# Kernel optimization log

Measured on AMD Instinct MI355X. Metric: run time of the kernel, lower is better.

## Reference

```python
import jax, jax.numpy as jnp
import numpy as np

D_MODEL = 1024
NUM_HEADS = 16
D_K = D_MODEL // NUM_HEADS


def setup_inputs() -> dict:
    key = jax.random.key(0)
    ks = jax.random.split(key, 12)
    B, T = 2, 2048
    s = 1.0 / np.sqrt(D_MODEL)
    inp = {
        "q": jax.random.normal(ks[0], (B, T, D_MODEL), jnp.float32),
        "k": jax.random.normal(ks[1], (B, T, D_MODEL), jnp.float32),
        "v": jax.random.normal(ks[2], (B, T, D_MODEL), jnp.float32),
        "mask": jnp.ones((B, 1, 1, T), dtype=bool),
        "Wq": jax.random.normal(ks[3], (D_MODEL, D_MODEL), jnp.float32) * s,
        "bq": jnp.zeros((D_MODEL,), jnp.float32),
        "Wk": jax.random.normal(ks[4], (D_MODEL, D_MODEL), jnp.float32) * s,
        "bk": jnp.zeros((D_MODEL,), jnp.float32),
        "Wv": jax.random.normal(ks[5], (D_MODEL, D_MODEL), jnp.float32) * s,
        "bv": jnp.zeros((D_MODEL,), jnp.float32),
        "Wo": jax.random.normal(ks[6], (D_MODEL, D_MODEL), jnp.float32) * s,
        "bo": jnp.zeros((D_MODEL,), jnp.float32),
    }
    return inp


def _split_heads(x):
    # (B, T, d_model) -> (B, H, T, d_k)
    B, T, _ = x.shape
    return x.reshape(B, T, NUM_HEADS, D_K).transpose(0, 2, 1, 3)


def reference(q, k, v, mask, Wq, bq, Wk, bk, Wv, bv, Wo, bo):
    B, Tq, _ = q.shape
    qh = _split_heads(q @ Wq + bq)   # (B,H,Tq,dk)
    kh = _split_heads(k @ Wk + bk)   # (B,H,Tk,dk)
    vh = _split_heads(v @ Wv + bv)   # (B,H,Tk,dk)
    scores = jnp.einsum("bhqd,bhkd->bhqk", qh, kh) / jnp.sqrt(jnp.float32(D_K))
    scores = jnp.where(mask, scores, -jnp.inf)
    attn = jax.nn.softmax(scores.astype(jnp.float32), axis=-1).astype(scores.dtype)
    # dropout is identity in eval mode
    out = jnp.einsum("bhqk,bhkd->bhqd", attn, vh)
    out = out.transpose(0, 2, 1, 3).reshape(B, Tq, D_MODEL)
    return out @ Wo + bo
```

## Files before the change

kernel.cpp:

```cpp
#include <hip/hip_runtime.h>
#include <hip/hip_bf16.h>


#define T_      2048
#define DMODEL  1024
#define NH      16
#define DK      64

typedef __attribute__((ext_vector_type(8))) short   bf16x8;
typedef __attribute__((ext_vector_type(4))) float   f32x4;
typedef __attribute__((ext_vector_type(4))) unsigned short u16x4;
typedef __attribute__((ext_vector_type(8))) unsigned short u16x8;

static __device__ __forceinline__ unsigned short f2bf(float f) {
    union { float f; unsigned u; } v; v.f = f;
    unsigned r = (v.u + 0x7fffu + ((v.u >> 16) & 1u)) >> 16;
    return (unsigned short)r;
}

static __device__ __forceinline__ void gld16(const unsigned short* g,
                                             unsigned short* l) {
    __builtin_amdgcn_global_load_lds(
        (const __attribute__((address_space(1))) unsigned int*)(const void*)g,
        (__attribute__((address_space(3))) unsigned int*)(void*)l, 16, 0, 0);
}

__global__ __launch_bounds__(256) void cast_x(
        const float* __restrict__ q, const float* __restrict__ k,
        const float* __restrict__ v, unsigned short* __restrict__ Xb) {
    const float* src = (blockIdx.y == 0) ? q : (blockIdx.y == 1) ? k : v;
    unsigned short* d = Xb + (size_t)blockIdx.y * (4096u * 1024u);
    size_t i = ((size_t)blockIdx.x * 256 + threadIdx.x) * 4;
    float4 vv = *reinterpret_cast<const float4*>(src + i);
    u16x4 o;
    o[0] = f2bf(vv.x); o[1] = f2bf(vv.y); o[2] = f2bf(vv.z); o[3] = f2bf(vv.w);
    *reinterpret_cast<u16x4*>(d + i) = o;
}

__global__ __launch_bounds__(256) void cast_wt(
        const float* __restrict__ Wq, const float* __restrict__ Wk,
        const float* __restrict__ Wv, const float* __restrict__ Wo,
        unsigned short* __restrict__ dst) {
    __shared__ unsigned short Ls[64][68];
    const float* src = (blockIdx.z == 0) ? Wq : (blockIdx.z == 1) ? Wk
                     : (blockIdx.z == 2) ? Wv : Wo;
    unsigned short* d = dst + (size_t)blockIdx.z * (1024u * 1024u);
    const int k0 = blockIdx.y * 64, n0 = blockIdx.x * 64;
    const int tid = threadIdx.x;
    #pragma unroll
    for (int i = 0; i < 4; i++) {
        int g = tid + i * 256;
        int r = g >> 4, c = (g & 15) * 4;
        float4 v = *reinterpret_cast<const float4*>(
            src + (size_t)(k0 + r) * 1024 + n0 + c);
        u16x4 o;
        o[0] = f2bf(v.x); o[1] = f2bf(v.y); o[2] = f2bf(v.z); o[3] = f2bf(v.w);
        *reinterpret_cast<u16x4*>(&Ls[r][c]) = o;
    }
    __syncthreads();
    #pragma unroll
    for (int i = 0; i < 4; i++) {
        int g = tid + i * 256;
        int n = g >> 4, kq = (g & 15) * 4;
        u16x4 o;
        #pragma unroll
        for (int j = 0; j < 4; j++) o[j] = Ls[kq + j][n];
        *reinterpret_cast<u16x4*>(d + (size_t)(n0 + n) * 1024 + k0 + kq) = o;
    }
}

#define CSCALE 0.18033688011112042f
#define CLD 136

__global__ __launch_bounds__(256) void qkv_gemm(
        const unsigned short* __restrict__ Xb,
        const unsigned short* __restrict__ Wt,
        const float* __restrict__ bq, const float* __restrict__ bk,
        const float* __restrict__ bv,
        unsigned short* __restrict__ Qh, unsigned short* __restrict__ Kf,
        unsigned short* __restrict__ Vf) {
    __shared__ unsigned short Al[128 * 32];
    __shared__ unsigned short Bl[128 * 32];
    __shared__ unsigned short Cl[128 * CLD];
    const int z = blockIdx.z;
    const unsigned short* X = Xb + (size_t)z * (4096u * 1024u);
    const unsigned short* W = Wt + (size_t)z * (1024u * 1024u);
    const float* bias = (z == 0) ? bq : (z == 1) ? bk : bv;
    const float oscale = (z == 0) ? CSCALE : 1.0f;

    const int tid  = threadIdx.x;
    const int lane = tid & 63, w = tid >> 6;
    const int quad = lane >> 4, l16 = lane & 15;
    const int row0 = blockIdx.y * 128, n0 = blockIdx.x * 128;
    const int wm = w >> 1, wn = w & 1;

    const int srow = w * 32 + (lane >> 2);
    const int scol = (lane & 3) * 8;
    const unsigned short* gA0 = X + (size_t)(row0 + srow) * 1024 + scol;
    const unsigned short* gA1 = gA0 + (size_t)16 * 1024;
    const unsigned short* gB0 = W + (size_t)(n0 + srow) * 1024 + scol;
    const unsigned short* gB1 = gB0 + (size_t)16 * 1024;
    unsigned short* lA0 = &Al[w * 1024];
    unsigned short* lA1 = &Al[w * 1024 + 512];
    unsigned short* lB0 = &Bl[w * 1024];
    unsigned short* lB1 = &Bl[w * 1024 + 512];

    f32x4 acc[4][4];
    for (int mt = 0; mt < 4; mt++)
        for (int nt = 0; nt < 4; nt++)
            acc[mt][nt] = (f32x4){0.f, 0.f, 0.f, 0.f};

    for (int k0 = 0; k0 < 1024; k0 += 32) {
        gld16(gA0 + k0, lA0);
        gld16(gA1 + k0, lA1);
        gld16(gB0 + k0, lB0);
        gld16(gB1 + k0, lB1);
        __syncthreads();
        bf16x8 a[4], b[4];
        #pragma unroll
        for (int mt = 0; mt < 4; mt++)
            a[mt] = *reinterpret_cast<const bf16x8*>(
                &Al[(wm * 64 + mt * 16 + l16) * 32 + quad * 8]);
        #pragma unroll
        for (int nt = 0; nt < 4; nt++)
            b[nt] = *reinterpret_cast<const bf16x8*>(
                &Bl[(wn * 64 + nt * 16 + l16) * 32 + quad * 8]);
        #pragma unroll
        for (int mt = 0; mt < 4; mt++)
            #pragma unroll
            for (int nt = 0; nt < 4; nt++)
                acc[mt][nt] = __builtin_amdgcn_mfma_f32_16x16x32_bf16(
                    a[mt], b[nt], acc[mt][nt], 0, 0, 0);
        __syncthreads();
    }

    #pragma unroll
    for (int mt = 0; mt < 4; mt++) {
        int row = wm * 64 + mt * 16 + quad * 4;
        #pragma unroll
        for (int nt = 0; nt < 4; nt++) {
            int col = wn * 64 + nt * 16 + l16;
            float bvv = bias[n0 + col];
            #pragma unroll
            for (int r = 0; r < 4; r++)
                Cl[(row + r) * CLD + col] = f2bf((acc[mt][nt][r] + bvv) * oscale);
        }
    }
    __syncthreads();

    const int bb = row0 >> 11;
    const int T0 = (row0 & 2047) >> 7;
    const int h0 = n0 >> 6;

    if (z == 0) {
        #pragma unroll
        for (int i = 0; i < 8; i++) {
            int c = tid + i * 256;
            int row = c >> 4, cc = (c & 15) * 8;
            int col = n0 + cc;
            int h = col >> 6, d = col & 63;
            int t = (row0 + row) & 2047;
            u16x8 vv = *reinterpret_cast<const u16x8*>(&Cl[row * CLD + cc]);
            *reinterpret_cast<u16x8*>(
                Qh + ((size_t)(bb * NH + h) * T_ + t) * DK + d) = vv;
        }
    } else if (z == 1) {
        #pragma unroll
        for (int i = 0; i < 8; i++) {
            int c = tid + i * 256;
            int hh = c >> 10;
            int nt = (c >> 7) & 7, kt = (c >> 6) & 1;
            int q4 = (c >> 4) & 3, lc = c & 15;
            int koff = (nt & 3) * 32 + (nt >> 2) * 4 + (lc >> 2) * 8 + (lc & 3);
            u16x8 vv = *reinterpret_cast<const u16x8*>(
                &Cl[koff * CLD + hh * 64 + kt * 32 + q4 * 8]);
            size_t base = ((size_t)((bb * NH + h0 + hh) * 16 + T0)) * 8192;
            *reinterpret_cast<u16x8*>(
                Kf + base + nt * 1024 + kt * 512 + q4 * 128 + lc * 8) = vv;
        }
    } else {
        #pragma unroll
        for (int i = 0; i < 8; i++) {
            int c = tid + i * 256;
            int hh = c >> 10;
            int kk = (c >> 8) & 3, nt = (c >> 6) & 3;
            int q4 = (c >> 4) & 3, lc = c & 15;
            int colc = hh * 64 + nt * 16 + lc;
            u16x8 vv;
            #pragma unroll
            for (int j = 0; j < 8; j++)
                vv[j] = Cl[(kk * 32 + q4 * 8 + j) * CLD + colc];
            size_t base = ((size_t)((bb * NH + h0 + hh) * 16 + T0)) * 8192;
            *reinterpret_cast<u16x8*>(
                Vf + base + kk * 2048 + nt * 512 + q4 * 128 + lc * 8) = vv;
        }
    }
}

__global__ __launch_bounds__(256, 4) void flash_attn(
        const unsigned short* __restrict__ Qh,
        const unsigned short* __restrict__ Kf,
        const unsigned short* __restrict__ Vf,
        float* __restrict__ Opart, float* __restrict__ Lpart) {
    __shared__ __attribute__((aligned(16))) unsigned short KV[16384];
    const int tid  = threadIdx.x;
    const int lane = tid & 63;
    const int w = tid >> 6;
    const int quad = lane >> 4, l16 = lane & 15;
    const int bh = blockIdx.y, b = bh >> 4, h = bh & 15;
    const int z = blockIdx.z;
    const int qrow = blockIdx.x * 128 + w * 32;
    const unsigned short* Qp = Qh + (size_t)bh * T_ * DK;
    float* Op = Opart + (size_t)z * 4096 * 1024;
    float* Lp = Lpart + (size_t)z * 32 * T_ + (size_t)bh * T_;

    bf16x8 qa[2][2];
    #pragma unroll
    for (int mt = 0; mt < 2; mt++)
        #pragma unroll
        for (int kt = 0; kt < 2; kt++)
            qa[mt][kt] = *reinterpret_cast<const bf16x8*>(
                Qp + (size_t)(qrow + mt * 16 + l16) * DK + kt * 32 + quad * 8);

    f32x4 o[2][4];
    float lsum[2] = {0.f, 0.f};
    #pragma unroll
    for (int mt = 0; mt < 2; mt++)
        #pragma unroll
        for (int nt = 0; nt < 4; nt++) o[mt][nt] = (f32x4){0.f, 0.f, 0.f, 0.f};

    const int halfsel = (w >> 1);
    unsigned short* lbase = &KV[halfsel * 8192 + (w & 1) * 4096];
    const size_t fragoff = ((w & 1) * 512) * 8 + (size_t)lane * 8;

    for (int it = 0; it < 8; it++) {
        const int T0 = z * 8 + it;
        const size_t winbase = ((size_t)(bh * 16 + T0)) * 8192;
        const unsigned short* gsrc =
            (halfsel == 0 ? Kf : Vf) + winbase + fragoff;
        __syncthreads();
        #pragma unroll
        for (int i = 0; i < 8; i++)
            gld16(gsrc + i * 512, lbase + i * 512);
        asm volatile("s_waitcnt vmcnt(0)" ::: "memory");
        __syncthreads();

        f32x4 s[2][8];
        #pragma unroll
        for (int nt = 0; nt < 8; nt++) {
            s[0][nt] = (f32x4){0.f, 0.f, 0.f, 0.f};
            s[1][nt] = (f32x4){0.f, 0.f, 0.f, 0.f};
        }
        #pragma unroll
        for (int nt = 0; nt < 8; nt++)
            #pragma unroll
            for (int kt = 0; kt < 2; kt++) {
                bf16x8 kbv = *reinterpret_cast<const bf16x8*>(
                    &KV[nt * 1024 + kt * 512 + lane * 8]);
                s[0][nt] = __builtin_amdgcn_mfma_f32_16x16x32_bf16(
                    kbv, qa[0][kt], s[0][nt], 0, 0, 0);
                s[1][nt] = __builtin_amdgcn_mfma_f32_16x16x32_bf16(
                    kbv, qa[1][kt], s[1][nt], 0, 0, 0);
            }

        int pk[2][16];
        #pragma unroll
        for (int mt = 0; mt < 2; mt++) {
            float lloc = 0.f;
            #pragma unroll
            for (int nt = 0; nt < 8; nt++) {
                float e0 = exp2f(s[mt][nt][0]);
                float e1 = exp2f(s[mt][nt][1]);
                float e2 = exp2f(s[mt][nt][2]);
                float e3 = exp2f(s[mt][nt][3]);
                int p0 = __builtin_amdgcn_perm(__float_as_int(e1),
                                               __float_as_int(e0), 0x07060302);
                int p1 = __builtin_amdgcn_perm(__float_as_int(e3),
                                               __float_as_int(e2), 0x07060302);
                pk[mt][nt * 2]     = p0;
                pk[mt][nt * 2 + 1] = p1;
                lloc += __int_as_float(p0 << 16) + __int_as_float(p0 & 0xffff0000)
                      + __int_as_float(p1 << 16) + __int_as_float(p1 & 0xffff0000);
            }
            lsum[mt] += lloc;
        }

        #pragma unroll
        for (int kt = 0; kt < 4; kt++) {
            union { int i[4]; bf16x8 v; } pu0, pu1;
            pu0.i[0] = pk[0][kt * 2];     pu0.i[1] = pk[0][kt * 2 + 1];
            pu0.i[2] = pk[0][kt * 2 + 8]; pu0.i[3] = pk[0][kt * 2 + 9];
            pu1.i[0] = pk[1][kt * 2];     pu1.i[1] = pk[1][kt * 2 + 1];
            pu1.i[2] = pk[1][kt * 2 + 8]; pu1.i[3] = pk[1][kt * 2 + 9];
            #pragma unroll
            for (int nt = 0; nt < 4; nt++) {
                bf16x8 vbv = *reinterpret_cast<const bf16x8*>(
                    &KV[8192 + kt * 2048 + nt * 512 + lane * 8]);
                o[0][nt] = __builtin_amdgcn_mfma_f32_16x16x32_bf16(
                    pu0.v, vbv, o[0][nt], 0, 0, 0);
                o[1][nt] = __builtin_amdgcn_mfma_f32_16x16x32_bf16(
                    pu1.v, vbv, o[1][nt], 0, 0, 0);
            }
        }
    }

    #pragma unroll
    for (int mt = 0; mt < 2; mt++) {
        float lf = lsum[mt];
        lf += __shfl_xor(lf, 16);
        lf += __shfl_xor(lf, 32);
        if (quad == 0) Lp[qrow + mt * 16 + l16] = lf;
        int t = qrow + mt * 16 + quad * 4;
        #pragma unroll
        for (int nt = 0; nt < 4; nt++) {
            int d = nt * 16 + l16;
            #pragma unroll
            for (int r = 0; r < 4; r++)
                Op[((size_t)(b * T_ + t + r)) * DMODEL + h * DK + d] = o[mt][nt][r];
        }
    }
}

__global__ __launch_bounds__(256) void combine(
        const float* __restrict__ O, const float* __restrict__ L,
        unsigned short* __restrict__ ctx) {
    size_t gid = (size_t)blockIdx.x * 256 + threadIdx.x;
    int row = (int)(gid >> 8);
    int c4  = (int)(gid & 255);
    int h = c4 >> 4;
    int b = row >> 11, t = row & 2047;
    size_t li = ((size_t)(b * 16 + h)) * T_ + t;
    float inv = 1.f / (L[li] + L[li + 32 * T_]);
    size_t oi = (size_t)row * 1024 + c4 * 4;
    float4 a  = *reinterpret_cast<const float4*>(O + oi);
    float4 c  = *reinterpret_cast<const float4*>(O + (size_t)4096 * 1024 + oi);
    u16x4 o;
    o[0] = f2bf((a.x + c.x) * inv);
    o[1] = f2bf((a.y + c.y) * inv);
    o[2] = f2bf((a.z + c.z) * inv);
    o[3] = f2bf((a.w + c.w) * inv);
    *reinterpret_cast<u16x4*>(ctx + oi) = o;
}

__global__ __launch_bounds__(256) void out_gemm(
        const unsigned short* __restrict__ A, const unsigned short* __restrict__ Wt,
        const float* __restrict__ bias, float* __restrict__ out) {
    __shared__ unsigned short Al[64 * 32];
    __shared__ unsigned short Bl[128 * 32];
    const int tid  = threadIdx.x;
    const int lane = tid & 63, w = tid >> 6;
    const int quad = lane >> 4, l16 = lane & 15;
    const int row0 = blockIdx.y * 64, n0 = blockIdx.x * 128;
    const int wm = w >> 1, wn = w & 1;

    const int scol = (lane & 3) * 8;
    const unsigned short* gA0 = A + (size_t)(row0 + w * 16 + (lane >> 2)) * 1024 + scol;
    const unsigned short* gB0 = Wt + (size_t)(n0 + w * 32 + (lane >> 2)) * 1024 + scol;
    const unsigned short* gB1 = gB0 + (size_t)16 * 1024;
    unsigned short* lA0 = &Al[w * 512];
    unsigned short* lB0 = &Bl[w * 1024];
    unsigned short* lB1 = &Bl[w * 1024 + 512];

    f32x4 acc[2][4];
    for (int mt = 0; mt < 2; mt++)
        for (int nt = 0; nt < 4; nt++)
            acc[mt][nt] = (f32x4){0.f, 0.f, 0.f, 0.f};

    for (int k0 = 0; k0 < 1024; k0 += 32) {
        gld16(gA0 + k0, lA0);
        gld16(gB0 + k0, lB0);
        gld16(gB1 + k0, lB1);
        __syncthreads();
        bf16x8 a[2], b[4];
        #pragma unroll
        for (int mt = 0; mt < 2; mt++)
            a[mt] = *reinterpret_cast<const bf16x8*>(
                &Al[(wm * 32 + mt * 16 + l16) * 32 + quad * 8]);
        #pragma unroll
        for (int nt = 0; nt < 4; nt++)
            b[nt] = *reinterpret_cast<const bf16x8*>(
                &Bl[(wn * 64 + nt * 16 + l16) * 32 + quad * 8]);
        #pragma unroll
        for (int mt = 0; mt < 2; mt++)
            #pragma unroll
            for (int nt = 0; nt < 4; nt++)
                acc[mt][nt] = __builtin_amdgcn_mfma_f32_16x16x32_bf16(
                    a[mt], b[nt], acc[mt][nt], 0, 0, 0);
        __syncthreads();
    }

    #pragma unroll
    for (int mt = 0; mt < 2; mt++) {
        int rowb = row0 + wm * 32 + mt * 16 + quad * 4;
        #pragma unroll
        for (int nt = 0; nt < 4; nt++) {
            int col = n0 + wn * 64 + nt * 16 + l16;
            float bvv = bias[col];
            #pragma unroll
            for (int r = 0; r < 4; r++)
                out[(size_t)(rowb + r) * 1024 + col] = acc[mt][nt][r] + bvv;
        }
    }
}

extern "C" void kernel_launch(void* const* d_in, const int* in_sizes, int n_in,
                              void* d_out, int out_size, void* d_ws, size_t ws_size,
                              hipStream_t stream) {
    const float* q  = (const float*)d_in[0];
    const float* k  = (const float*)d_in[1];
    const float* v  = (const float*)d_in[2];
    const float* Wq = (const float*)d_in[4];
    const float* bq = (const float*)d_in[5];
    const float* Wk = (const float*)d_in[6];
    const float* bk = (const float*)d_in[7];
    const float* Wv = (const float*)d_in[8];
    const float* bv = (const float*)d_in[9];
    const float* Wo = (const float*)d_in[10];
    const float* bo = (const float*)d_in[11];
    float* out = (float*)d_out;

    unsigned short* ws  = (unsigned short*)d_ws;
    unsigned short* Wt  = ws;
    unsigned short* Qh  = ws + (size_t)4  * 1024 * 1024;
    unsigned short* Kf  = ws + (size_t)8  * 1024 * 1024;
    unsigned short* Vf  = ws + (size_t)12 * 1024 * 1024;
    unsigned short* Xb  = ws + (size_t)16 * 1024 * 1024;
    float* Opart = (float*)(ws + (size_t)16 * 1024 * 1024);
    float* Lpart = (float*)(ws + (size_t)32 * 1024 * 1024);
    unsigned short* ctx = Kf;

    cast_x <<<dim3(4096, 3), 256, 0, stream>>>(q, k, v, Xb);
    cast_wt<<<dim3(16, 16, 4), 256, 0, stream>>>(Wq, Wk, Wv, Wo, Wt);
    qkv_gemm<<<dim3(8, 32, 3), 256, 0, stream>>>(Xb, Wt, bq, bk, bv, Qh, Kf, Vf);
    flash_attn<<<dim3(16, 32, 2), 256, 0, stream>>>(Qh, Kf, Vf, Opart, Lpart);
    combine<<<dim3(4096), 256, 0, stream>>>(Opart, Lpart, ctx);
    out_gemm<<<dim3(8, 64), 256, 0, stream>>>(ctx, Wt + (size_t)3 * 1048576, bo, out);
}
```

Before: 246.2 us.

## Fuse cast kernels, fold split-K combine into output GEMM, MFMA row sums

Merges the activation and weight cast kernels into one launch, removes the separate combine kernel by having the output GEMM read both fp32 partial outputs, normalise by the inverse denominator and convert to bf16 while staging its A tile, and computes the softmax denominator in flash attention with an MFMA against a ones vector instead of scalar adds and shuffles. The aim is to cut launches and the ctx round-trip through global memory. In exchange, the out GEMM now reads fp32 partials directly, 8x per column tile (eight column blocks reread the same rows), so it moves more data than the bf16 ctx it replaces.

```diff
diff --git a/kernel.cpp b/kernel.cpp
--- a/kernel.cpp
+++ b/kernel.cpp
@@ -25,47 +25,50 @@
         (__attribute__((address_space(3))) unsigned int*)(void*)l, 16, 0, 0);
 }
 
-__global__ __launch_bounds__(256) void cast_x(
+__global__ __launch_bounds__(256) void prep(
         const float* __restrict__ q, const float* __restrict__ k,
-        const float* __restrict__ v, unsigned short* __restrict__ Xb) {
-    const float* src = (blockIdx.y == 0) ? q : (blockIdx.y == 1) ? k : v;
-    unsigned short* d = Xb + (size_t)blockIdx.y * (4096u * 1024u);
-    size_t i = ((size_t)blockIdx.x * 256 + threadIdx.x) * 4;
-    float4 vv = *reinterpret_cast<const float4*>(src + i);
-    u16x4 o;
-    o[0] = f2bf(vv.x); o[1] = f2bf(vv.y); o[2] = f2bf(vv.z); o[3] = f2bf(vv.w);
-    *reinterpret_cast<u16x4*>(d + i) = o;
-}
-
-__global__ __launch_bounds__(256) void cast_wt(
+        const float* __restrict__ v,
         const float* __restrict__ Wq, const float* __restrict__ Wk,
         const float* __restrict__ Wv, const float* __restrict__ Wo,
-        unsigned short* __restrict__ dst) {
+        unsigned short* __restrict__ Xb, unsigned short* __restrict__ Wt) {
     __shared__ unsigned short Ls[64][68];
-    const float* src = (blockIdx.z == 0) ? Wq : (blockIdx.z == 1) ? Wk
-                     : (blockIdx.z == 2) ? Wv : Wo;
-    unsigned short* d = dst + (size_t)blockIdx.z * (1024u * 1024u);
-    const int k0 = blockIdx.y * 64, n0 = blockIdx.x * 64;
-    const int tid = threadIdx.x;
-    #pragma unroll
-    for (int i = 0; i < 4; i++) {
-        int g = tid + i * 256;
-        int r = g >> 4, c = (g & 15) * 4;
-        float4 v = *reinterpret_cast<const float4*>(
-            src + (size_t)(k0 + r) * 1024 + n0 + c);
+    const int bx = blockIdx.x, tid = threadIdx.x;
+    if (bx < 12288) {
+        int y = bx >> 12, sub = bx & 4095;
+        const float* src = (y == 0) ? q : (y == 1) ? k : v;
+        unsigned short* d = Xb + (size_t)y * (4096u * 1024u);
+        size_t i = ((size_t)sub * 256 + tid) * 4;
+        float4 vv = *reinterpret_cast<const float4*>(src + i);
         u16x4 o;
-        o[0] = f2bf(v.x); o[1] = f2bf(v.y); o[2] = f2bf(v.z); o[3] = f2bf(v.w);
-        *reinterpret_cast<u16x4*>(&Ls[r][c]) = o;
-    }
-    __syncthreads();
-    #pragma unroll
-    for (int i = 0; i < 4; i++) {
-        int g = tid + i * 256;
-        int n = g >> 4, kq = (g & 15) * 4;
-        u16x4 o;
-        #pragma unroll
-        for (int j = 0; j < 4; j++) o[j] = Ls[kq + j][n];
-        *reinterpret_cast<u16x4*>(d + (size_t)(n0 + n) * 1024 + k0 + kq) = o;
+        o[0] = f2bf(vv.x); o[1] = f2bf(vv.y); o[2] = f2bf(vv.z); o[3] = f2bf(vv.w);
+        *reinterpret_cast<u16x4*>(d + i) = o;
+    } else {
+        int bxx = bx - 12288;
+        int zz = bxx >> 8, rem = bxx & 255;
+        int k0 = (rem >> 4) * 64, n0 = (rem & 15) * 64;
+        const float* src = (zz == 0) ? Wq : (zz == 1) ? Wk
+                         : (zz == 2) ? Wv : Wo;
+        unsigned short* d = Wt + (size_t)zz * (1024u * 1024u);
+        #pragma unroll
+        for (int i = 0; i < 4; i++) {
+            int g = tid + i * 256;
+            int r = g >> 4, c = (g & 15) * 4;
+            float4 vv = *reinterpret_cast<const float4*>(
+                src + (size_t)(k0 + r) * 1024 + n0 + c);
+            u16x4 o;
+            o[0] = f2bf(vv.x); o[1] = f2bf(vv.y); o[2] = f2bf(vv.z); o[3] = f2bf(vv.w);
+            *reinterpret_cast<u16x4*>(&Ls[r][c]) = o;
+        }
+        __syncthreads();
+        #pragma unroll
+        for (int i = 0; i < 4; i++) {
+            int g = tid + i * 256;
+            int n = g >> 4, kq = (g & 15) * 4;
+            u16x4 o;
+            #pragma unroll
+            for (int j = 0; j < 4; j++) o[j] = Ls[kq + j][n];
+            *reinterpret_cast<u16x4*>(d + (size_t)(n0 + n) * 1024 + k0 + kq) = o;
+        }
     }
 }
 
@@ -222,12 +225,16 @@
             qa[mt][kt] = *reinterpret_cast<const bf16x8*>(
                 Qp + (size_t)(qrow + mt * 16 + l16) * DK + kt * 32 + quad * 8);
 
-    f32x4 o[2][4];
-    float lsum[2] = {0.f, 0.f};
-    #pragma unroll
-    for (int mt = 0; mt < 2; mt++)
+    f32x4 o[2][4], lden[2];
+    #pragma unroll
+    for (int mt = 0; mt < 2; mt++) {
+        lden[mt] = (f32x4){0.f, 0.f, 0.f, 0.f};
         #pragma unroll
         for (int nt = 0; nt < 4; nt++) o[mt][nt] = (f32x4){0.f, 0.f, 0.f, 0.f};
+    }
+
+    union { unsigned u[4]; bf16x8 v; } ones;
+    ones.u[0] = ones.u[1] = ones.u[2] = ones.u[3] = 0x3F803F80u;
 
     const int halfsel = (w >> 1);
     unsigned short* lbase = &KV[halfsel * 8192 + (w & 1) * 4096];
@@ -265,25 +272,18 @@
 
         int pk[2][16];
         #pragma unroll
-        for (int mt = 0; mt < 2; mt++) {
-            float lloc = 0.f;
+        for (int mt = 0; mt < 2; mt++)
             #pragma unroll
             for (int nt = 0; nt < 8; nt++) {
                 float e0 = exp2f(s[mt][nt][0]);
                 float e1 = exp2f(s[mt][nt][1]);
                 float e2 = exp2f(s[mt][nt][2]);
                 float e3 = exp2f(s[mt][nt][3]);
-                int p0 = __builtin_amdgcn_perm(__float_as_int(e1),
-                                               __float_as_int(e0), 0x07060302);
-                int p1 = __builtin_amdgcn_perm(__float_as_int(e3),
-                                               __float_as_int(e2), 0x07060302);
-                pk[mt][nt * 2]     = p0;
-                pk[mt][nt * 2 + 1] = p1;
-                lloc += __int_as_float(p0 << 16) + __int_as_float(p0 & 0xffff0000)
-                      + __int_as_float(p1 << 16) + __int_as_float(p1 & 0xffff0000);
+                pk[mt][nt * 2] = __builtin_amdgcn_perm(
+                    __float_as_int(e1), __float_as_int(e0), 0x07060302);
+                pk[mt][nt * 2 + 1] = __builtin_amdgcn_perm(
+                    __float_as_int(e3), __float_as_int(e2), 0x07060302);
             }
-            lsum[mt] += lloc;
-        }
 
         #pragma unroll
         for (int kt = 0; kt < 4; kt++) {
@@ -301,15 +301,20 @@
                 o[1][nt] = __builtin_amdgcn_mfma_f32_16x16x32_bf16(
                     pu1.v, vbv, o[1][nt], 0, 0, 0);
             }
+            lden[0] = __builtin_amdgcn_mfma_f32_16x16x32_bf16(
+                pu0.v, ones.v, lden[0], 0, 0, 0);
+            lden[1] = __builtin_amdgcn_mfma_f32_16x16x32_bf16(
+                pu1.v, ones.v, lden[1], 0, 0, 0);
         }
     }
 
     #pragma unroll
     for (int mt = 0; mt < 2; mt++) {
-        float lf = lsum[mt];
-        lf += __shfl_xor(lf, 16);
-        lf += __shfl_xor(lf, 32);
-        if (quad == 0) Lp[qrow + mt * 16 + l16] = lf;
+        if (l16 == 0) {
+            #pragma unroll
+            for (int r = 0; r < 4; r++)
+                Lp[qrow + mt * 16 + quad * 4 + r] = lden[mt][r];
+        }
         int t = qrow + mt * 16 + quad * 4;
         #pragma unroll
         for (int nt = 0; nt < 4; nt++) {
@@ -321,43 +326,34 @@
     }
 }
 
-__global__ __launch_bounds__(256) void combine(
-        const float* __restrict__ O, const float* __restrict__ L,
-        unsigned short* __restrict__ ctx) {
-    size_t gid = (size_t)blockIdx.x * 256 + threadIdx.x;
-    int row = (int)(gid >> 8);
-    int c4  = (int)(gid & 255);
-    int h = c4 >> 4;
-    int b = row >> 11, t = row & 2047;
-    size_t li = ((size_t)(b * 16 + h)) * T_ + t;
-    float inv = 1.f / (L[li] + L[li + 32 * T_]);
-    size_t oi = (size_t)row * 1024 + c4 * 4;
-    float4 a  = *reinterpret_cast<const float4*>(O + oi);
-    float4 c  = *reinterpret_cast<const float4*>(O + (size_t)4096 * 1024 + oi);
-    u16x4 o;
-    o[0] = f2bf((a.x + c.x) * inv);
-    o[1] = f2bf((a.y + c.y) * inv);
-    o[2] = f2bf((a.z + c.z) * inv);
-    o[3] = f2bf((a.w + c.w) * inv);
-    *reinterpret_cast<u16x4*>(ctx + oi) = o;
-}
-
 __global__ __launch_bounds__(256) void out_gemm(
-        const unsigned short* __restrict__ A, const unsigned short* __restrict__ Wt,
+        const float* __restrict__ Opart, const float* __restrict__ Lpart,
+        const unsigned short* __restrict__ Wt,
         const float* __restrict__ bias, float* __restrict__ out) {
     __shared__ unsigned short Al[64 * 32];
     __shared__ unsigned short Bl[128 * 32];
+    __shared__ float invs[64 * 16];
     const int tid  = threadIdx.x;
     const int lane = tid & 63, w = tid >> 6;
     const int quad = lane >> 4, l16 = lane & 15;
     const int row0 = blockIdx.y * 64, n0 = blockIdx.x * 128;
     const int wm = w >> 1, wn = w & 1;
 
+    #pragma unroll
+    for (int i = 0; i < 4; i++) {
+        int e = tid + i * 256;
+        int row = e >> 4, hh = e & 15;
+        int rg = row0 + row, bb = rg >> 11, tt = rg & 2047;
+        size_t li = ((size_t)(bb * NH + hh)) * T_ + tt;
+        invs[e] = 1.f / (Lpart[li] + Lpart[li + 32 * T_]);
+    }
+
     const int scol = (lane & 3) * 8;
-    const unsigned short* gA0 = A + (size_t)(row0 + w * 16 + (lane >> 2)) * 1024 + scol;
+    const int arow = w * 16 + (lane >> 2);
+    const float* gO0 = Opart + (size_t)(row0 + arow) * 1024 + scol;
+    const float* gO1 = gO0 + (size_t)4096 * 1024;
     const unsigned short* gB0 = Wt + (size_t)(n0 + w * 32 + (lane >> 2)) * 1024 + scol;
     const unsigned short* gB1 = gB0 + (size_t)16 * 1024;
-    unsigned short* lA0 = &Al[w * 512];
     unsigned short* lB0 = &Bl[w * 1024];
     unsigned short* lB1 = &Bl[w * 1024 + 512];
 
@@ -366,10 +362,28 @@
         for (int nt = 0; nt < 4; nt++)
             acc[mt][nt] = (f32x4){0.f, 0.f, 0.f, 0.f};
 
+    __syncthreads();
+
     for (int k0 = 0; k0 < 1024; k0 += 32) {
-        gld16(gA0 + k0, lA0);
         gld16(gB0 + k0, lB0);
         gld16(gB1 + k0, lB1);
+        {
+            float iv = invs[arow * 16 + (k0 >> 6)];
+            float4 x0 = *reinterpret_cast<const float4*>(gO0 + k0);
+            float4 x1 = *reinterpret_cast<const float4*>(gO0 + k0 + 4);
+            float4 y0 = *reinterpret_cast<const float4*>(gO1 + k0);
+            float4 y1 = *reinterpret_cast<const float4*>(gO1 + k0 + 4);
+            u16x8 vv;
+            vv[0] = f2bf((x0.x + y0.x) * iv);
+            vv[1] = f2bf((x0.y + y0.y) * iv);
+            vv[2] = f2bf((x0.z + y0.z) * iv);
+            vv[3] = f2bf((x0.w + y0.w) * iv);
+            vv[4] = f2bf((x1.x + y1.x) * iv);
+            vv[5] = f2bf((x1.y + y1.y) * iv);
+            vv[6] = f2bf((x1.z + y1.z) * iv);
+            vv[7] = f2bf((x1.w + y1.w) * iv);
+            *reinterpret_cast<u16x8*>(&Al[arow * 32 + scol]) = vv;
+        }
         __syncthreads();
         bf16x8 a[2], b[4];
         #pragma unroll
@@ -427,12 +441,10 @@
     unsigned short* Xb  = ws + (size_t)16 * 1024 * 1024;
     float* Opart = (float*)(ws + (size_t)16 * 1024 * 1024);
     float* Lpart = (float*)(ws + (size_t)32 * 1024 * 1024);
-    unsigned short* ctx = Kf;
-
-    cast_x <<<dim3(4096, 3), 256, 0, stream>>>(q, k, v, Xb);
-    cast_wt<<<dim3(16, 16, 4), 256, 0, stream>>>(Wq, Wk, Wv, Wo, Wt);
+
+    prep<<<dim3(13312), 256, 0, stream>>>(q, k, v, Wq, Wk, Wv, Wo, Xb, Wt);
     qkv_gemm<<<dim3(8, 32, 3), 256, 0, stream>>>(Xb, Wt, bq, bk, bv, Qh, Kf, Vf);
     flash_attn<<<dim3(16, 32, 2), 256, 0, stream>>>(Qh, Kf, Vf, Opart, Lpart);
-    combine<<<dim3(4096), 256, 0, stream>>>(Opart, Lpart, ctx);
-    out_gemm<<<dim3(8, 64), 256, 0, stream>>>(ctx, Wt + (size_t)3 * 1048576, bo, out);
-}
+    out_gemm<<<dim3(8, 64), 256, 0, stream>>>(Opart, Lpart,
+                                              Wt + (size_t)3 * 1048576, bo, out);
+}
```

Result: slower. 261.9 us (+6.3%).
